# Kernel optimization log

Hardware: AMD Instinct MI355X
Metric: run time of the kernel (lower is better)

## Reference

```python
import jax, jax.numpy as jnp
import numpy as np

BS, SEQ, HID = 2, 2048, 1024
HEADS, BLOCK = 16, 64
HEAD_DIM = HID // HEADS


def setup_inputs() -> dict:
    key = jax.random.key(0)
    ks = jax.random.split(key, 5)
    s = 1.0 / np.sqrt(HID)
    return {
        "hidden_states": jax.random.normal(ks[0], (BS, SEQ, HID), jnp.float32),
        "Wq": jax.random.normal(ks[1], (HID, HID), jnp.float32) * s,
        "bq": jnp.zeros((HID,), jnp.float32),
        "Wk": jax.random.normal(ks[2], (HID, HID), jnp.float32) * s,
        "bk": jnp.zeros((HID,), jnp.float32),
        "Wv": jax.random.normal(ks[3], (HID, HID), jnp.float32) * s,
        "bv": jnp.zeros((HID,), jnp.float32),
        "Wo": jax.random.normal(ks[4], (HID, HID), jnp.float32) * s,
        "bo": jnp.zeros((HID,), jnp.float32),
    }


def reference(hidden_states, Wq, bq, Wk, bk, Wv, bv, Wo, bo):
    b, s, _ = hidden_states.shape
    # torch Linear: y = x @ W.T + b
    q = (hidden_states @ Wq.T + bq).reshape(b, s, HEADS, HEAD_DIM)
    k = (hidden_states @ Wk.T + bk).reshape(b, s, HEADS, HEAD_DIM)
    v = (hidden_states @ Wv.T + bv).reshape(b, s, HEADS, HEAD_DIM)
    scale = 1.0 / np.sqrt(HEAD_DIM).astype(np.float32)
    scores = jnp.einsum("bqhd,bkhd->bhqk", q, k) * scale  # [B,H,S,S]
    # block-level causal mask: kv block index <= query block index
    blk = jnp.arange(s) // BLOCK
    mask = blk[None, :] <= blk[:, None]  # [S,S]
    scores = jnp.where(mask[None, None], scores, jnp.finfo(scores.dtype).min)
    attn = jax.nn.softmax(scores, axis=-1)
    out = jnp.einsum("bhqk,bkhd->bqhd", attn, v).reshape(b, s, HID)
    return out @ Wo.T + bo
```

## Files before the change

### kernel.cpp

```cpp
#include <hip/hip_runtime.h>

#define BS 2
#define SEQ 2048
#define HID 1024
#define HEADS 16
#define HDIM 64
#define MTOT (BS * SEQ)

#define QSCALE 0.18033688f

typedef __bf16 bf16x8 __attribute__((ext_vector_type(8)));
typedef float floatx4 __attribute__((ext_vector_type(4)));
typedef short short8 __attribute__((ext_vector_type(8)));
typedef unsigned short u16x4 __attribute__((ext_vector_type(4)));
typedef unsigned int u32x2 __attribute__((ext_vector_type(2)));
typedef unsigned int u32x4 __attribute__((ext_vector_type(4)));
typedef unsigned int uint2v __attribute__((ext_vector_type(2)));

__device__ __forceinline__ floatx4 mfma16x16x32bf16(short8 a, short8 b, floatx4 c) {
    return __builtin_amdgcn_mfma_f32_16x16x32_bf16(
        __builtin_bit_cast(bf16x8, a), __builtin_bit_cast(bf16x8, b), c, 0, 0, 0);
}

__device__ __forceinline__ unsigned short f2bf(float f) {
    unsigned int u = __builtin_bit_cast(unsigned int, f);
    u += 0x7fffu + ((u >> 16) & 1u);
    return (unsigned short)(u >> 16);
}

__device__ __forceinline__ unsigned int cvt_pk_bf16(float lo, float hi) {
    unsigned int r;
    asm("v_cvt_pk_bf16_f32 %0, %1, %2" : "=v"(r) : "v"(lo), "v"(hi));
    return r;
}

__device__ __forceinline__ float fast_exp2(float x) {
#if __has_builtin(__builtin_amdgcn_exp2f)
    return __builtin_amdgcn_exp2f(x);
#else
    return __expf(x * 0.6931471805599453f);
#endif
}

__device__ __forceinline__ uint2v pl16_swap(unsigned int a, unsigned int b) {
#if __has_builtin(__builtin_amdgcn_permlane16_swap)
    return __builtin_amdgcn_permlane16_swap(a, b, 0, 0);
#else
    unsigned int x, y;
    asm("v_mov_b32 %0, %2\n\t"
        "v_mov_b32 %1, %3\n\t"
        "v_permlane16_swap_b32 %0, %1"
        : "=&v"(x), "=&v"(y) : "v"(a), "v"(b));
    uint2v r; r[0] = x; r[1] = y; return r;
#endif
}
__device__ __forceinline__ uint2v pl32_swap(unsigned int a, unsigned int b) {
#if __has_builtin(__builtin_amdgcn_permlane32_swap)
    return __builtin_amdgcn_permlane32_swap(a, b, 0, 0);
#else
    unsigned int x, y;
    asm("v_mov_b32 %0, %2\n\t"
        "v_mov_b32 %1, %3\n\t"
        "v_permlane32_swap_b32 %0, %1"
        : "=&v"(x), "=&v"(y) : "v"(a), "v"(b));
    uint2v r; r[0] = x; r[1] = y; return r;
#endif
}

#define GLOAD_LDS16(gsrc, ldst)                                                   \
    __builtin_amdgcn_global_load_lds(                                             \
        (const __attribute__((address_space(1))) void*)(gsrc),                    \
        (__attribute__((address_space(3))) void*)(ldst), 16, 0, 0)

__global__ __launch_bounds__(256) void cvt5(
    const float* __restrict__ X, const float* __restrict__ Wq,
    const float* __restrict__ Wk, const float* __restrict__ Wv,
    const float* __restrict__ Wo, unsigned short* __restrict__ dst)
{
    const int y = blockIdx.y;
    const float* src = (y == 0) ? X : (y == 1) ? Wq : (y == 2) ? Wk : (y == 3) ? Wv : Wo;
    const size_t base = (y == 0) ? 0 : (size_t)(4u << 20) + (size_t)(y - 1) * (1u << 20);
    const int n4 = (y == 0) ? (1 << 20) : (1 << 18);
    const float scale = (y == 1) ? QSCALE : 1.0f;
    int i = blockIdx.x * 256 + threadIdx.x;
    if (i >= n4) return;
    floatx4 v = *(const floatx4*)(src + (size_t)i * 4);
    v *= scale;
    unsigned int p0 = (unsigned int)f2bf(v[0]) | ((unsigned int)f2bf(v[1]) << 16);
    unsigned int p1 = (unsigned int)f2bf(v[2]) | ((unsigned int)f2bf(v[3]) << 16);
    u32x2 pk = {p0, p1};
    *(u32x2*)(dst + base + (size_t)i * 4) = pk;
}

__global__ __launch_bounds__(256) void gemm_qkv(
    const unsigned short* __restrict__ X,
    const unsigned short* __restrict__ W0, const unsigned short* __restrict__ W1,
    const unsigned short* __restrict__ W2,
    const float* __restrict__ B0, const float* __restrict__ B1,
    const float* __restrict__ B2,
    unsigned short* __restrict__ out_bf)
{
    __shared__ __align__(16) unsigned short sA[64 * 32];
    __shared__ __align__(16) unsigned short sB[3][128 * 32];

    const int tid  = threadIdx.x;
    const int m0   = blockIdx.x * 64;
    const int n0   = blockIdx.y * 128;
    const int lane = tid & 63, w = tid >> 6;
    const int l16  = lane & 15, grp = lane >> 4;
    const int wm   = w & 1, wn = w >> 1;

    const unsigned short* Wz[3] = {W0, W1, W2};

    floatx4 acc[3][2][4];
#pragma unroll
    for (int z = 0; z < 3; ++z)
#pragma unroll
        for (int i = 0; i < 2; ++i)
#pragma unroll
            for (int j = 0; j < 4; ++j) acc[z][i][j] = (floatx4){0.f, 0.f, 0.f, 0.f};

    auto stage = [&](int kb) {
        const int kcol = kb * 32;
        {
            int row = tid >> 2, c8 = (tid & 3) * 8;
            GLOAD_LDS16(X + (size_t)(m0 + row) * HID + kcol + c8, &sA[tid * 8]);
        }
#pragma unroll
        for (int i = 0; i < 6; ++i) {
            int g2 = tid + i * 256;
            int z = g2 >> 9, g3 = g2 & 511;
            int row = g3 >> 2, c8 = (g3 & 3) * 8;
            GLOAD_LDS16(Wz[z] + (size_t)(n0 + row) * HID + kcol + c8, &sB[z][g3 * 8]);
        }
    };

    stage(0);
    for (int kb = 0; kb < 32; ++kb) {
        __syncthreads();
        short8 af[2], bfr[3][4];
#pragma unroll
        for (int t = 0; t < 2; ++t)
            af[t] = *(const short8*)&sA[(wm * 32 + t * 16 + l16) * 32 + grp * 8];
#pragma unroll
        for (int z = 0; z < 3; ++z)
#pragma unroll
            for (int t = 0; t < 4; ++t)
                bfr[z][t] = *(const short8*)&sB[z][(wn * 64 + t * 16 + l16) * 32 + grp * 8];
        __syncthreads();
        if (kb + 1 < 32) stage(kb + 1);
#pragma unroll
        for (int mt = 0; mt < 2; ++mt)
#pragma unroll
            for (int nt = 0; nt < 4; ++nt) {
                acc[0][mt][nt] = mfma16x16x32bf16(bfr[0][nt], af[mt], acc[0][mt][nt]);
                acc[1][mt][nt] = mfma16x16x32bf16(bfr[1][nt], af[mt], acc[1][mt][nt]);
                acc[2][mt][nt] = mfma16x16x32bf16(af[mt], bfr[2][nt], acc[2][mt][nt]);
            }
    }

    const int hidx = (n0 + wn * 64) >> 6;
    {
#pragma unroll
        for (int nt = 0; nt < 4; ++nt) {
            int dbase = nt * 16 + grp * 4;
            floatx4 b4 = *(const floatx4*)&B0[n0 + wn * 64 + dbase];
            b4 *= QSCALE;
#pragma unroll
            for (int mt = 0; mt < 2; ++mt) {
                int m = m0 + wm * 32 + mt * 16 + l16;
                int bidx = m >> 11, s = m & (SEQ - 1);
                u32x2 pk;
                pk[0] = cvt_pk_bf16(acc[0][mt][nt][0] + b4[0], acc[0][mt][nt][1] + b4[1]);
                pk[1] = cvt_pk_bf16(acc[0][mt][nt][2] + b4[2], acc[0][mt][nt][3] + b4[3]);
                *(u32x2*)&out_bf[
                    ((((size_t)bidx * HEADS + hidx) * SEQ + s) * HDIM + dbase)] = pk;
            }
        }
    }
    {
        const size_t outz = (size_t)MTOT * HID;
        const int bidx = m0 >> 11;
        const int kvb  = (m0 & (SEQ - 1)) >> 6;
        const size_t hbase = outz + ((size_t)bidx * HEADS + hidx) * SEQ * HDIM;
        const int grpf = grp >> 1, j0 = (grp & 1) * 4;
#pragma unroll
        for (int nt = 0; nt < 4; ++nt) {
            floatx4 b4 = *(const floatx4*)&B1[n0 + wn * 64 + nt * 16 + grp * 4];
#pragma unroll
            for (int mt = 0; mt < 2; ++mt) {
                u32x2 pk;
                pk[0] = cvt_pk_bf16(acc[1][mt][nt][0] + b4[0], acc[1][mt][nt][1] + b4[1]);
                pk[1] = cvt_pk_bf16(acc[1][mt][nt][2] + b4[2], acc[1][mt][nt][3] + b4[3]);
                size_t F = hbase
                    + (size_t)((((kvb * 4 + (wm * 2 + mt)) * 2 + (nt >> 1)) * 512)
                    + ((((nt & 1) * 2 + grpf) * 16 + l16) * 8) + j0);
                *(u32x2*)&out_bf[F] = pk;
            }
        }
    }
    {
        const size_t outz = (size_t)2 * ((size_t)MTOT * HID);
        const int bidx = m0 >> 11;
        const int kvb  = (m0 & (SEQ - 1)) >> 6;
        const size_t hbase = outz + ((size_t)bidx * HEADS + hidx) * SEQ * HDIM;
        const int j0 = (grp & 1) * 4;
#pragma unroll
        for (int nt = 0; nt < 4; ++nt) {
            float bias = B2[n0 + wn * 64 + nt * 16 + l16];
#pragma unroll
            for (int mt = 0; mt < 2; ++mt) {
                u32x2 pk;
                pk[0] = cvt_pk_bf16(acc[2][mt][nt][0] + bias, acc[2][mt][nt][1] + bias);
                pk[1] = cvt_pk_bf16(acc[2][mt][nt][2] + bias, acc[2][mt][nt][3] + bias);
                size_t F = hbase + (size_t)((((kvb * 4 + nt) * 2 + wm) * 512)
                    + (((mt * 2 + (grp >> 1)) * 16 + l16) * 8) + j0);
                *(u32x2*)&out_bf[F] = pk;
            }
        }
    }
}

template <int BM, int BN>
__global__ __launch_bounds__(256) void gemm_out(
    const unsigned short* __restrict__ X, const unsigned short* __restrict__ W,
    const float* __restrict__ Bb, float* __restrict__ out_f)
{
    constexpr int MT = BM / 32, NT = BN / 32;
    constexpr int NCH = (BM + BN) * 4;
    __shared__ __align__(16) unsigned short sA[BM * 32];
    __shared__ __align__(16) unsigned short sB[BN * 32];

    const int tid  = threadIdx.x;
    const int m0   = blockIdx.x * BM;
    const int n0   = blockIdx.y * BN;
    const int lane = tid & 63, w = tid >> 6;
    const int l16  = lane & 15, grp = lane >> 4;
    const int wm   = w & 1, wn = w >> 1;

    floatx4 acc[MT][NT];
#pragma unroll
    for (int i = 0; i < MT; ++i)
#pragma unroll
        for (int j = 0; j < NT; ++j) acc[i][j] = (floatx4){0.f, 0.f, 0.f, 0.f};

    auto stage = [&](int kb) {
        const int kcol = kb * 32;
#pragma unroll
        for (int i = 0; i < NCH / 256; ++i) {
            int g = tid + i * 256;
            if (g < BM * 4) {
                int row = g >> 2, c8 = (g & 3) * 8;
                GLOAD_LDS16(X + (size_t)(m0 + row) * HID + kcol + c8, &sA[g * 8]);
            } else {
                int g2 = g - BM * 4;
                int row = g2 >> 2, c8 = (g2 & 3) * 8;
                GLOAD_LDS16(W + (size_t)(n0 + row) * HID + kcol + c8, &sB[g2 * 8]);
            }
        }
    };

    stage(0);
    for (int kb = 0; kb < 32; ++kb) {
        __syncthreads();
        short8 af[MT], bfr[NT];
#pragma unroll
        for (int t = 0; t < MT; ++t)
            af[t] = *(const short8*)&sA[(wm * (BM / 2) + t * 16 + l16) * 32 + grp * 8];
#pragma unroll
        for (int t = 0; t < NT; ++t)
            bfr[t] = *(const short8*)&sB[(wn * (BN / 2) + t * 16 + l16) * 32 + grp * 8];
        __syncthreads();
        if (kb + 1 < 32) stage(kb + 1);
#pragma unroll
        for (int mt = 0; mt < MT; ++mt)
#pragma unroll
            for (int nt = 0; nt < NT; ++nt)
                acc[mt][nt] = mfma16x16x32bf16(af[mt], bfr[nt], acc[mt][nt]);
    }

#pragma unroll
    for (int nt = 0; nt < NT; ++nt) {
        int n = n0 + wn * (BN / 2) + nt * 16 + l16;
        float bias = Bb[n];
#pragma unroll
        for (int mt = 0; mt < MT; ++mt)
#pragma unroll
            for (int r = 0; r < 4; ++r) {
                int m = m0 + wm * (BM / 2) + mt * 16 + grp * 4 + r;
                out_f[(size_t)m * HID + n] = acc[mt][nt][r] + bias;
            }
    }
}

__global__ __launch_bounds__(512) void attn_kernel(
    const unsigned short* __restrict__ Qw, const unsigned short* __restrict__ Kf,
    const unsigned short* __restrict__ Vf, unsigned short* __restrict__ X2)
{
    const int wg = blockIdx.x;
    const int xcd = wg & 7, k = wg >> 3;
    const int bh  = (k >> 4) * 8 + xcd;
    const int pairj = k & 15;
    const int tid = threadIdx.x;
    const int wid = tid >> 6;
    const int quarter = wid & 3;
    const int half = wid >> 2;
    const int qblk = half ? (31 - pairj) : pairj;
    const int b = bh >> 4, h = bh & 15;

    const int lane = tid & 63;
    const int l16  = lane & 15, grp = lane >> 4;

    const size_t head = ((size_t)b * HEADS + h) * (size_t)SEQ * HDIM;
    const unsigned short* Kh = Kf + head;
    const unsigned short* Vh = Vf + head;

    short8 ka[4][2], kbuf[4][2], vf[4][2];

    auto loadK = [&](short8 (&kf)[4][2], int kb) {
#pragma unroll
        for (int nt = 0; nt < 4; ++nt)
#pragma unroll
            for (int ks = 0; ks < 2; ++ks)
                kf[nt][ks] = *(const short8*)(Kh +
                    (size_t)(((kb * 4 + nt) * 2 + ks) * 512) + lane * 8);
    };

    const int nkb = qblk + 1;
    const int q0  = qblk * 64 + quarter * 16;

    short8 qf[2];
#pragma unroll
    for (int ks = 0; ks < 2; ++ks)
        qf[ks] = *(const short8*)(Qw + head +
            (size_t)(q0 + l16) * HDIM + ks * 32 + grp * 8);

    floatx4 o[4];
#pragma unroll
    for (int i = 0; i < 4; ++i) o[i] = (floatx4){0.f, 0.f, 0.f, 0.f};
    float li = 0.f;

    auto process = [&](short8 (&kfc)[4][2], short8 (&kfn)[4][2], int kb) {
        {
#pragma unroll
            for (int nt = 0; nt < 4; ++nt)
#pragma unroll
                for (int ks = 0; ks < 2; ++ks)
                    vf[nt][ks] = *(const short8*)(Vh +
                        (size_t)(((kb * 4 + nt) * 2 + ks) * 512) + lane * 8);
        }
        floatx4 sv[4];
        __builtin_amdgcn_s_setprio(1);
#pragma unroll
        for (int nt = 0; nt < 4; ++nt) {
            floatx4 zz = (floatx4){0.f, 0.f, 0.f, 0.f};
            zz = mfma16x16x32bf16(kfc[nt][0], qf[0], zz);
            zz = mfma16x16x32bf16(kfc[nt][1], qf[1], zz);
            sv[nt] = zz;
        }
        __builtin_amdgcn_s_setprio(0);
        if (kb + 1 < nkb) loadK(kfn, kb + 1);

        float rs = 0.f;
#pragma unroll
        for (int nt = 0; nt < 4; ++nt) {
            floatx4 p;
#pragma unroll
            for (int r = 0; r < 4; ++r) p[r] = fast_exp2(sv[nt][r]);
            sv[nt] = p;
            rs += (p[0] + p[1]) + (p[2] + p[3]);
        }
        li += rs;

        unsigned int ap[4][2];
#pragma unroll
        for (int nt = 0; nt < 4; ++nt) {
            ap[nt][0] = cvt_pk_bf16(sv[nt][0], sv[nt][1]);
            ap[nt][1] = cvt_pk_bf16(sv[nt][2], sv[nt][3]);
        }
        uint2v t0 = pl32_swap(ap[0][0], ap[1][0]);
        uint2v t1 = pl32_swap(ap[0][1], ap[1][1]);
        uint2v s0 = pl16_swap(t0[0], t0[1]);
        uint2v s1 = pl16_swap(t1[0], t1[1]);
        u32x4 f0 = {s0[0], s1[0], s0[1], s1[1]};
        uint2v t2 = pl32_swap(ap[2][0], ap[3][0]);
        uint2v t3 = pl32_swap(ap[2][1], ap[3][1]);
        uint2v s2 = pl16_swap(t2[0], t2[1]);
        uint2v s3 = pl16_swap(t3[0], t3[1]);
        u32x4 f1 = {s2[0], s3[0], s2[1], s3[1]};
        short8 pf0 = __builtin_bit_cast(short8, f0);
        short8 pf1 = __builtin_bit_cast(short8, f1);

        __builtin_amdgcn_s_setprio(1);
#pragma unroll
        for (int dt = 0; dt < 4; ++dt) {
            o[dt] = mfma16x16x32bf16(vf[dt][0], pf0, o[dt]);
            o[dt] = mfma16x16x32bf16(vf[dt][1], pf1, o[dt]);
        }
        __builtin_amdgcn_s_setprio(0);
    };

    loadK(ka, 0);
    int kb = 0;
    while (true) {
        process(ka, kbuf, kb);
        if (++kb >= nkb) break;
        process(kbuf, ka, kb);
        if (++kb >= nkb) break;
    }

    li += __shfl_xor(li, 16);
    li += __shfl_xor(li, 32);

    float inv = 1.0f / li;
    int srow = q0 + l16;
#pragma unroll
    for (int dt = 0; dt < 4; ++dt) {
        u32x2 pk;
        pk[0] = cvt_pk_bf16(o[dt][0] * inv, o[dt][1] * inv);
        pk[1] = cvt_pk_bf16(o[dt][2] * inv, o[dt][3] * inv);
        *(u32x2*)&X2[((size_t)b * SEQ + srow) * HID +
                     h * HDIM + dt * 16 + grp * 4] = pk;
    }
}

extern "C" void kernel_launch(void* const* d_in, const int* in_sizes, int n_in,
                              void* d_out, int out_size, void* d_ws, size_t ws_size,
                              hipStream_t stream) {
    int iX, iWq, ibq, iWk, ibk, iWv, ibv, iWo, ibo;
    if (in_sizes[0] == MTOT * HID) {
        iX = 0; iWq = 1; ibq = 2; iWk = 3; ibk = 4; iWv = 5; ibv = 6; iWo = 7; ibo = 8;
    } else {
        iWk = 0; iWo = 1; iWq = 2; iWv = 3; ibk = 4; ibo = 5; ibq = 6; ibv = 7; iX = 8;
    }
    const float* X  = (const float*)d_in[iX];
    const float* Wq = (const float*)d_in[iWq];
    const float* bq = (const float*)d_in[ibq];
    const float* Wk = (const float*)d_in[iWk];
    const float* bk = (const float*)d_in[ibk];
    const float* Wv = (const float*)d_in[iWv];
    const float* bv = (const float*)d_in[ibv];
    const float* Wo = (const float*)d_in[iWo];
    const float* bo = (const float*)d_in[ibo];
    float* out = (float*)d_out;

    unsigned short* ws = (unsigned short*)d_ws;
    const size_t T = (size_t)MTOT * HID;
    unsigned short* qw  = ws;
    unsigned short* kfr = ws + T;
    unsigned short* vfr = ws + 2 * T;
    unsigned short* x2  = ws + 3 * T;
    unsigned short* Xb  = ws + 4 * T;
    unsigned short* Wqb = Xb + T;
    unsigned short* Wkb = Wqb + (size_t)HID * HID;
    unsigned short* Wvb = Wkb + (size_t)HID * HID;
    unsigned short* Wob = Wvb + (size_t)HID * HID;

    cvt5<<<dim3(4096, 5), 256, 0, stream>>>(X, Wq, Wk, Wv, Wo, Xb);
    gemm_qkv<<<dim3(64, 8), 256, 0, stream>>>(
        Xb, Wqb, Wkb, Wvb, bq, bk, bv, qw);
    attn_kernel<<<dim3(512), 512, 0, stream>>>(qw, kfr, vfr, x2);
    gemm_out<64, 128><<<dim3(64, 8), 256, 0, stream>>>(x2, Wob, bo, out);
}
```

Measured before the change: 187.2 us.

## Process two 16-row query tiles per wave in attention to reuse K/V fragments

The attention kernel now launches 256 threads (4 waves) instead of 512, and each wave handles 32 query rows as two 16-row tiles sharing the same K and V register fragments. This halves the global loads of K/V per query row and gives more independent MFMA work per wave to hide latency. In exchange it raises register pressure (two sets of accumulators and scores) and lowers the number of waves available for latency hiding.

```diff
diff --git a/kernel.cpp b/kernel.cpp
--- a/kernel.cpp
+++ b/kernel.cpp
@@ -293,7 +293,7 @@
     }
 }
 
-__global__ __launch_bounds__(512) void attn_kernel(
+__global__ __launch_bounds__(256) void attn_kernel(
     const unsigned short* __restrict__ Qw, const unsigned short* __restrict__ Kf,
     const unsigned short* __restrict__ Vf, unsigned short* __restrict__ X2)
 {
@@ -303,8 +303,8 @@
     const int pairj = k & 15;
     const int tid = threadIdx.x;
     const int wid = tid >> 6;
-    const int quarter = wid & 3;
-    const int half = wid >> 2;
+    const int q2   = wid & 1;
+    const int half = wid >> 1;
     const int qblk = half ? (31 - pairj) : pairj;
     const int b = bh >> 4, h = bh & 15;
 
@@ -327,51 +327,26 @@
     };
 
     const int nkb = qblk + 1;
-    const int q0  = qblk * 64 + quarter * 16;
-
-    short8 qf[2];
-#pragma unroll
-    for (int ks = 0; ks < 2; ++ks)
-        qf[ks] = *(const short8*)(Qw + head +
+    const int q0  = qblk * 64 + q2 * 32;
+
+    short8 qfA[2], qfB[2];
+#pragma unroll
+    for (int ks = 0; ks < 2; ++ks) {
+        qfA[ks] = *(const short8*)(Qw + head +
             (size_t)(q0 + l16) * HDIM + ks * 32 + grp * 8);
-
-    floatx4 o[4];
-#pragma unroll
-    for (int i = 0; i < 4; ++i) o[i] = (floatx4){0.f, 0.f, 0.f, 0.f};
-    float li = 0.f;
-
-    auto process = [&](short8 (&kfc)[4][2], short8 (&kfn)[4][2], int kb) {
-        {
-#pragma unroll
-            for (int nt = 0; nt < 4; ++nt)
-#pragma unroll
-                for (int ks = 0; ks < 2; ++ks)
-                    vf[nt][ks] = *(const short8*)(Vh +
-                        (size_t)(((kb * 4 + nt) * 2 + ks) * 512) + lane * 8);
-        }
-        floatx4 sv[4];
-        __builtin_amdgcn_s_setprio(1);
-#pragma unroll
-        for (int nt = 0; nt < 4; ++nt) {
-            floatx4 zz = (floatx4){0.f, 0.f, 0.f, 0.f};
-            zz = mfma16x16x32bf16(kfc[nt][0], qf[0], zz);
-            zz = mfma16x16x32bf16(kfc[nt][1], qf[1], zz);
-            sv[nt] = zz;
-        }
-        __builtin_amdgcn_s_setprio(0);
-        if (kb + 1 < nkb) loadK(kfn, kb + 1);
-
-        float rs = 0.f;
-#pragma unroll
-        for (int nt = 0; nt < 4; ++nt) {
-            floatx4 p;
-#pragma unroll
-            for (int r = 0; r < 4; ++r) p[r] = fast_exp2(sv[nt][r]);
-            sv[nt] = p;
-            rs += (p[0] + p[1]) + (p[2] + p[3]);
-        }
-        li += rs;
-
+        qfB[ks] = *(const short8*)(Qw + head +
+            (size_t)(q0 + 16 + l16) * HDIM + ks * 32 + grp * 8);
+    }
+
+    floatx4 oA[4], oB[4];
+#pragma unroll
+    for (int i = 0; i < 4; ++i) {
+        oA[i] = (floatx4){0.f, 0.f, 0.f, 0.f};
+        oB[i] = (floatx4){0.f, 0.f, 0.f, 0.f};
+    }
+    float liA = 0.f, liB = 0.f;
+
+    auto cascade = [&](floatx4 (&sv)[4], short8& pf0, short8& pf1) {
         unsigned int ap[4][2];
 #pragma unroll
         for (int nt = 0; nt < 4; ++nt) {
@@ -388,14 +363,72 @@
         uint2v s2 = pl16_swap(t2[0], t2[1]);
         uint2v s3 = pl16_swap(t3[0], t3[1]);
         u32x4 f1 = {s2[0], s3[0], s2[1], s3[1]};
-        short8 pf0 = __builtin_bit_cast(short8, f0);
-        short8 pf1 = __builtin_bit_cast(short8, f1);
-
+        pf0 = __builtin_bit_cast(short8, f0);
+        pf1 = __builtin_bit_cast(short8, f1);
+    };
+
+    auto process = [&](short8 (&kfc)[4][2], short8 (&kfn)[4][2], int kb) {
+        {
+#pragma unroll
+            for (int nt = 0; nt < 4; ++nt)
+#pragma unroll
+                for (int ks = 0; ks < 2; ++ks)
+                    vf[nt][ks] = *(const short8*)(Vh +
+                        (size_t)(((kb * 4 + nt) * 2 + ks) * 512) + lane * 8);
+        }
+        floatx4 svA[4], svB[4];
         __builtin_amdgcn_s_setprio(1);
 #pragma unroll
+        for (int nt = 0; nt < 4; ++nt) {
+            floatx4 za = (floatx4){0.f, 0.f, 0.f, 0.f};
+            za = mfma16x16x32bf16(kfc[nt][0], qfA[0], za);
+            za = mfma16x16x32bf16(kfc[nt][1], qfA[1], za);
+            svA[nt] = za;
+            floatx4 zb = (floatx4){0.f, 0.f, 0.f, 0.f};
+            zb = mfma16x16x32bf16(kfc[nt][0], qfB[0], zb);
+            zb = mfma16x16x32bf16(kfc[nt][1], qfB[1], zb);
+            svB[nt] = zb;
+        }
+        __builtin_amdgcn_s_setprio(0);
+        if (kb + 1 < nkb) loadK(kfn, kb + 1);
+
+        float rsA = 0.f;
+#pragma unroll
+        for (int nt = 0; nt < 4; ++nt) {
+            floatx4 p;
+#pragma unroll
+            for (int r = 0; r < 4; ++r) p[r] = fast_exp2(svA[nt][r]);
+            svA[nt] = p;
+            rsA += (p[0] + p[1]) + (p[2] + p[3]);
+        }
+        liA += rsA;
+        short8 pfA0, pfA1;
+        cascade(svA, pfA0, pfA1);
+        __builtin_amdgcn_s_setprio(1);
+#pragma unroll
         for (int dt = 0; dt < 4; ++dt) {
-            o[dt] = mfma16x16x32bf16(vf[dt][0], pf0, o[dt]);
-            o[dt] = mfma16x16x32bf16(vf[dt][1], pf1, o[dt]);
+            oA[dt] = mfma16x16x32bf16(vf[dt][0], pfA0, oA[dt]);
+            oA[dt] = mfma16x16x32bf16(vf[dt][1], pfA1, oA[dt]);
+        }
+        __builtin_amdgcn_s_setprio(0);
+
+        float rsB = 0.f;
+#pragma unroll
+        for (int nt = 0; nt < 4; ++nt) {
+            floatx4 p;
+#pragma unroll
+            for (int r = 0; r < 4; ++r) p[r] = fast_exp2(svB[nt][r]);
+            svB[nt] = p;
+            rsB += (p[0] + p[1]) + (p[2] + p[3]);
+        }
+        liB += rsB;
+        short8 pfB0, pfB1;
+        cascade(svB, pfB0, pfB1);
+        __builtin_amdgcn_s_setprio(1);
+#pragma unroll
+        for (int dt = 0; dt < 4; ++dt) {
+            oB[dt] = mfma16x16x32bf16(vf[dt][0], pfB0, oB[dt]);
+            oB[dt] = mfma16x16x32bf16(vf[dt][1], pfB1, oB[dt]);
         }
         __builtin_amdgcn_s_setprio(0);
     };
@@ -409,18 +442,35 @@
         if (++kb >= nkb) break;
     }
 
-    li += __shfl_xor(li, 16);
-    li += __shfl_xor(li, 32);
-
-    float inv = 1.0f / li;
-    int srow = q0 + l16;
-#pragma unroll
-    for (int dt = 0; dt < 4; ++dt) {
-        u32x2 pk;
-        pk[0] = cvt_pk_bf16(o[dt][0] * inv, o[dt][1] * inv);
-        pk[1] = cvt_pk_bf16(o[dt][2] * inv, o[dt][3] * inv);
-        *(u32x2*)&X2[((size_t)b * SEQ + srow) * HID +
-                     h * HDIM + dt * 16 + grp * 4] = pk;
+    {
+        float l = liA;
+        l += __shfl_xor(l, 16);
+        l += __shfl_xor(l, 32);
+        float inv = 1.0f / l;
+        int srow = q0 + l16;
+#pragma unroll
+        for (int dt = 0; dt < 4; ++dt) {
+            u32x2 pk;
+            pk[0] = cvt_pk_bf16(oA[dt][0] * inv, oA[dt][1] * inv);
+            pk[1] = cvt_pk_bf16(oA[dt][2] * inv, oA[dt][3] * inv);
+            *(u32x2*)&X2[((size_t)b * SEQ + srow) * HID +
+                         h * HDIM + dt * 16 + grp * 4] = pk;
+        }
+    }
+    {
+        float l = liB;
+        l += __shfl_xor(l, 16);
+        l += __shfl_xor(l, 32);
+        float inv = 1.0f / l;
+        int srow = q0 + 16 + l16;
+#pragma unroll
+        for (int dt = 0; dt < 4; ++dt) {
+            u32x2 pk;
+            pk[0] = cvt_pk_bf16(oB[dt][0] * inv, oB[dt][1] * inv);
+            pk[1] = cvt_pk_bf16(oB[dt][2] * inv, oB[dt][3] * inv);
+            *(u32x2*)&X2[((size_t)b * SEQ + srow) * HID +
+                         h * HDIM + dt * 16 + grp * 4] = pk;
+        }
     }
 }
 
@@ -459,6 +509,6 @@
     cvt5<<<dim3(4096, 5), 256, 0, stream>>>(X, Wq, Wk, Wv, Wo, Xb);
     gemm_qkv<<<dim3(64, 8), 256, 0, stream>>>(
         Xb, Wqb, Wkb, Wvb, bq, bk, bv, qw);
-    attn_kernel<<<dim3(512), 512, 0, stream>>>(qw, kfr, vfr, x2);
+    attn_kernel<<<dim3(512), 256, 0, stream>>>(qw, kfr, vfr, x2);
     gemm_out<64, 128><<<dim3(64, 8), 256, 0, stream>>>(x2, Wob, bo, out);
 }
```

New measurement: 197.4 us. 1.05x slower.
